# Kernel optimization log

Hardware: AMD Instinct MI355X
Metric: run time of the kernel (lower is better)

Reference implementation:

```python
import jax, jax.numpy as jnp
import numpy as np
from jax import lax


def setup_inputs() -> dict:
    key = jax.random.key(0)
    k1, k2 = jax.random.split(key)
    B, N, D = 4, 4096, 128
    f_s = jax.random.normal(k1, (B, N, D), dtype=jnp.float32)
    f_trans = jax.random.normal(k2, (B, N, D), dtype=jnp.float32)
    return {"f_s": f_s, "f_trans": f_trans}


def reference(f_s, f_trans):
    temp = 10.0
    eps = 1e-8
    B, N, D = f_s.shape
    # pairwise dot products, reused for cosine sim and for the logits ("all")
    dots = jnp.einsum('bnd,bmd->bnm', f_s, f_trans)  # [B,N,M]
    norm_s = jnp.linalg.norm(f_s, axis=-1)       # [B,N]
    norm_t = jnp.linalg.norm(f_trans, axis=-1)   # [B,M]
    # torch.cosine_similarity: dot / max(|x|*|y|, eps)
    sim = dots / jnp.maximum(norm_s[:, :, None] * norm_t[:, None, :], eps)
    # argmax over dim=1 (the N axis) -> index per (b, m)
    idx = jnp.argmax(sim, axis=1)  # [B,M] int
    # gather f_trans rows at those indices (detached in the original via numpy)
    pos_q_trans = lax.stop_gradient(
        jnp.take_along_axis(f_trans, idx[..., None], axis=1))  # [B,M,D]
    pos_logit = jnp.sum(f_s * pos_q_trans, axis=-1) / temp  # [B,N] (N==M)
    pos_exp = jnp.exp(pos_logit)
    # sum_m exp(<f_s_n, f_trans_m>/temp) without materializing [B,N,M,D]
    all_exp = jnp.sum(jnp.exp(dots / temp), axis=-1)  # [B,N]
    ratio = jnp.clip(pos_exp / all_exp, 1e-40)
    loss = jnp.mean(jnp.sum(-jnp.log(ratio), axis=-1) / N)
    return loss
```

## Files before the change

### kernel.cpp

```cpp
#include <hip/hip_runtime.h>
#include <math.h>

#define BB 4
#define NN 4096
#define DD 128
#define HS 8
#define NIT 8
#define QG 32

typedef __attribute__((ext_vector_type(8))) short bf16x8;
typedef __attribute__((ext_vector_type(4))) float f32x4;

__device__ __forceinline__ void mfma_16x16x32_bf16(f32x4& d, bf16x8 a, bf16x8 b) {
  asm volatile("v_mfma_f32_16x16x32_bf16 %0, %1, %2, %0" : "+v"(d) : "v"(a), "v"(b));
}

__device__ __forceinline__ void gload16(const void* g, void* lds) {
  __builtin_amdgcn_global_load_lds(
      (const __attribute__((address_space(1))) void*)g,
      (__attribute__((address_space(3))) void*)lds, 16, 0, 0);
}

__device__ __forceinline__ float vexp2(float x) {
  float r; asm("v_exp_f32 %0, %1" : "=v"(r) : "v"(x)); return r;
}

__device__ __forceinline__ unsigned short f2b(float x) {
  union { float f; unsigned u; } v; v.f = x;
  unsigned r = v.u + 0x7fffu + ((v.u >> 16) & 1u);
  return (unsigned short)(r >> 16);
}

__global__ __launch_bounds__(256) void k_prep(const float* __restrict__ fs,
                                              const float* __restrict__ ft,
                                              unsigned* __restrict__ outb,
                                              float* __restrict__ inv_norm) {
  int w = threadIdx.x >> 6, lane = threadIdx.x & 63;
  int row = blockIdx.x * 4 + w;
  bool is_s = row < BB * NN;
  const float* src = is_s ? fs + (size_t)row * DD
                          : ft + ((size_t)row - BB * NN) * DD;
  float2 v = ((const float2*)src)[lane];
  const float C = 0.14426950408889634f;
  float cx = is_s ? v.x : v.x * C;
  float cy = is_s ? v.y : v.y * C;
  outb[(size_t)row * 64 + lane] = ((unsigned)f2b(cy) << 16) | f2b(cx);
  if (is_s) {
    float s = v.x * v.x + v.y * v.y;
#pragma unroll
    for (int off = 32; off > 0; off >>= 1) s += __shfl_xor(s, off);
    if (lane == 0) inv_norm[row] = 1.0f / sqrtf(s);
  }
}

__global__ __launch_bounds__(256, 4) void k_main(const unsigned short* __restrict__ fsb,
                                                 const unsigned short* __restrict__ ftb,
                                                 const float* __restrict__ inv_norm,
                                                 float* __restrict__ psum,
                                                 float2* __restrict__ pmax) {
  __shared__ __align__(16) char smem[40960];
  float* psb = (float*)(smem + 32768);

  const int t = threadIdx.x;
  const int w = t >> 6, lane = t & 63;
  const int l15 = lane & 15, g = lane >> 4;
  const int bid = blockIdx.x;
  const int q = bid & 31, h = (bid >> 5) & 7, b = bid >> 8;
  const int m0 = q * 128 + w * 32;

  const int srcThr = ((t >> 4) << 8) + (((t & 15) ^ ((t >> 4) & 15)) << 4);
  const int ldsThr = w * 1024;

  const unsigned short* Ab = ftb + ((size_t)b * NN + m0) * DD;
  bf16x8 af[4][2];
#pragma unroll
  for (int kk = 0; kk < 4; kk++)
#pragma unroll
    for (int mf = 0; mf < 2; mf++)
      af[kk][mf] = *(const bf16x8*)(Ab + (mf * 16 + l15) * DD + kk * 32 + g * 8);

  const char* gB0 = (const char*)(fsb + ((size_t)b * NN + h * 512) * DD);
  const float* invb = inv_norm + (size_t)b * NN + h * 512;

  char* cb = smem;
  char* nb = smem + 16384;

#pragma unroll
  for (int p = 0; p < 4; p++)
    gload16(gB0 + p * 4096 + srcThr, cb + p * 4096 + ldsThr);

  float bkey[2][4];
#pragma unroll
  for (int mf = 0; mf < 2; mf++)
#pragma unroll
    for (int j = 0; j < 4; j++) bkey[mf][j] = 0.0f;

#pragma unroll 1
  for (int it = 0; it < NIT; ++it) {
    __syncthreads();
    if (it + 1 < NIT) {
      const char* gBn = gB0 + (it + 1) * 16384;
#pragma unroll
      for (int p = 0; p < 4; p++)
        gload16(gBn + p * 4096 + srcThr, nb + p * 4096 + ldsThr);
    }
    float svn[4];
#pragma unroll
    for (int fj = 0; fj < 4; fj++) svn[fj] = invb[it * 64 + fj * 16 + l15];

    f32x4 acc[2][4] = {};
#pragma unroll
    for (int kk = 0; kk < 4; kk++) {
      bf16x8 bf[4];
#pragma unroll
      for (int fj = 0; fj < 4; fj++)
        bf[fj] = *(const bf16x8*)(cb + (fj * 16 + l15) * 256 + (((kk * 4 + g) ^ l15) << 4));
#pragma unroll
      for (int mf = 0; mf < 2; mf++)
#pragma unroll
        for (int fj = 0; fj < 4; fj++)
          mfma_16x16x32_bf16(acc[mf][fj], af[kk][mf], bf[fj]);
    }

#pragma unroll
    for (int fj = 0; fj < 4; fj++) {
      float e0 = vexp2(acc[0][fj][0]), e1 = vexp2(acc[0][fj][1]);
      float e2 = vexp2(acc[0][fj][2]), e3 = vexp2(acc[0][fj][3]);
      float e4 = vexp2(acc[1][fj][0]), e5 = vexp2(acc[1][fj][1]);
      float e6 = vexp2(acc[1][fj][2]), e7 = vexp2(acc[1][fj][3]);
      float s = ((e0 + e1) + (e2 + e3)) + ((e4 + e5) + (e6 + e7));
      s += __shfl_xor(s, 16);
      s += __shfl_xor(s, 32);
      if (g == 0) psb[w * 512 + it * 64 + fj * 16 + l15] = s;
    }
    const unsigned codebase = (unsigned)((7 - it) << 2);
#pragma unroll
    for (int fj = 0; fj < 4; fj++) {
      const unsigned code = codebase | (unsigned)(3 - fj);
#pragma unroll
      for (int mf = 0; mf < 2; mf++)
#pragma unroll
        for (int j = 0; j < 4; j++) {
          float v = fmaf(acc[mf][fj][j], svn[fj], 4.0f);
          unsigned kb = (__float_as_uint(v) & 0xFFFFFFE0u) | code;
          bkey[mf][j] = fmaxf(bkey[mf][j], __uint_as_float(kb));
        }
    }
    char* tmp = cb; cb = nb; nb = tmp;
  }
  __syncthreads();

#pragma unroll
  for (int rr = 0; rr < 2; rr++) {
    int nl = rr * 256 + t;
    float s4 = (psb[nl] + psb[512 + nl]) + (psb[1024 + nl] + psb[1536 + nl]);
    psum[((size_t)(b * QG + q)) * NN + h * 512 + nl] = s4;
  }

#pragma unroll
  for (int mf = 0; mf < 2; mf++)
#pragma unroll
    for (int j = 0; j < 4; j++) {
      unsigned bits = __float_as_uint(bkey[mf][j]);
      unsigned code = bits & 31u;
      int itw = 7 - (int)(code >> 2);
      int fjw = 3 - (int)(code & 3u);
      int n = h * 512 + itw * 64 + fjw * 16 + l15;
      float vq = __uint_as_float(bits & 0xFFFFFFE0u);
#pragma unroll
      for (int off = 1; off <= 8; off <<= 1) {
        float ov = __shfl_xor(vq, off);
        int   on = __shfl_xor(n, off);
        if (ov > vq || (ov == vq && on < n)) { vq = ov; n = on; }
      }
      if (l15 == 0) {
        int m = m0 + mf * 16 + g * 4 + j;
        float2 pr; pr.x = vq; pr.y = __int_as_float(n);
        pmax[((size_t)b * NN + m) * HS + h] = pr;
      }
    }
}

__global__ __launch_bounds__(256) void k_post(const float* __restrict__ fs,
                                              const float* __restrict__ ft,
                                              const float* __restrict__ psum,
                                              const float2* __restrict__ pmax,
                                              float* __restrict__ blockpart) {
  __shared__ float part[4];
  int w = threadIdx.x >> 6, lane = threadIdx.x & 63;
  int row = blockIdx.x * 4 + w;
  int b = row >> 12, pn = row & (NN - 1);
  float v = -INFINITY; int i = 0x7fffffff;
  if (lane < HS) {
    float2 pm = pmax[(size_t)row * HS + lane];
    v = pm.x; i = __float_as_int(pm.y);
  }
#pragma unroll
  for (int off = 1; off <= 4; off <<= 1) {
    float ov = __shfl_xor(v, off);
    int   oi = __shfl_xor(i, off);
    if (ov > v || (ov == v && oi < i)) { v = ov; i = oi; }
  }
  int j = __shfl(i, 0);
  float tot = (lane < QG) ? psum[((size_t)(b * QG + lane)) * NN + pn] : 0.0f;
#pragma unroll
  for (int off = 1; off <= 16; off <<= 1) tot += __shfl_xor(tot, off);
  float2 a = ((const float2*)(fs + (size_t)row * DD))[lane];
  float2 c = ((const float2*)(ft + ((size_t)b * NN + j) * DD))[lane];
  float s = a.x * c.x + a.y * c.y;
#pragma unroll
  for (int off = 32; off > 0; off >>= 1) s += __shfl_xor(s, off);
  if (lane == 0) {
    float term = logf(tot) - s * 0.1f;
    part[w] = fminf(term, 92.103403719761827f);
  }
  __syncthreads();
  if (threadIdx.x == 0)
    blockpart[blockIdx.x] = part[0] + part[1] + part[2] + part[3];
}

__global__ __launch_bounds__(256) void k_final(const float* __restrict__ blockpart,
                                               float* __restrict__ out) {
  __shared__ float red[256];
  float s = 0.0f;
  for (int i = threadIdx.x; i < (BB * NN) / 4; i += 256) s += blockpart[i];
  red[threadIdx.x] = s;
  __syncthreads();
  for (int st = 128; st > 0; st >>= 1) {
    if (threadIdx.x < st) red[threadIdx.x] += red[threadIdx.x + st];
    __syncthreads();
  }
  if (threadIdx.x == 0) out[0] = red[0] * (1.0f / (BB * NN));
}

extern "C" void kernel_launch(void* const* d_in, const int* in_sizes, int n_in,
                              void* d_out, int out_size, void* d_ws, size_t ws_size,
                              hipStream_t stream) {
  const float* fs = (const float*)d_in[0];
  const float* ft = (const float*)d_in[1];
  float* out = (float*)d_out;

  const size_t NE = (size_t)BB * NN * DD;
  unsigned short* fsb = (unsigned short*)d_ws;
  unsigned short* ftb = fsb + NE;
  float*  inv_norm = (float*)(ftb + NE);
  float*  psum     = inv_norm + (size_t)BB * NN;
  float2* pmax     = (float2*)(psum + (size_t)BB * QG * NN);
  float*  blockpart = (float*)(pmax + (size_t)BB * NN * HS);

  k_prep<<<(2 * BB * NN) / 4, 256, 0, stream>>>(fs, ft, (unsigned*)fsb, inv_norm);
  k_main<<<BB * HS * QG, 256, 0, stream>>>(fsb, ftb, inv_norm, psum, pmax);
  k_post<<<(BB * NN) / 4, 256, 0, stream>>>(fs, ft, psum, pmax, blockpart);
  k_final<<<1, 256, 0, stream>>>(blockpart, out);
}
```

Measured before the change: 54.41 us.

## Split N range into 16 slices, drop LDS psum reduction, vectorize prep

The main kernel now splits the N dimension into 16 slices of 256 instead of 8 of 512, doubling the grid to 2048 blocks with half the iterations each. It raises the launch-bounds occupancy hint to 5 and shrinks LDS to 32 KB. Per-wave exp partial sums go straight to a [B,N,128] global buffer instead of being reduced through LDS, and the post kernel reduces 128 partials per row. The prep kernel uses float4 loads with both inputs per thread, and inverse norms are hoisted out of the loop. The trade is more parallelism and fewer barriers against more global partial-sum traffic and scattered strided writes.

```diff
diff --git a/kernel.cpp b/kernel.cpp
--- a/kernel.cpp
+++ b/kernel.cpp
@@ -4,12 +4,14 @@
 #define BB 4
 #define NN 4096
 #define DD 128
-#define HS 8
-#define NIT 8
+#define HS 16
+#define NIT 4
 #define QG 32
+#define NPS 128
 
 typedef __attribute__((ext_vector_type(8))) short bf16x8;
 typedef __attribute__((ext_vector_type(4))) float f32x4;
+typedef __attribute__((ext_vector_type(4))) unsigned short u16x4;
 
 __device__ __forceinline__ void mfma_16x16x32_bf16(f32x4& d, bf16x8 a, bf16x8 b) {
   asm volatile("v_mfma_f32_16x16x32_bf16 %0, %1, %2, %0" : "+v"(d) : "v"(a), "v"(b));
@@ -33,39 +35,36 @@
 
 __global__ __launch_bounds__(256) void k_prep(const float* __restrict__ fs,
                                               const float* __restrict__ ft,
-                                              unsigned* __restrict__ outb,
+                                              unsigned short* __restrict__ fsb,
+                                              unsigned short* __restrict__ ftb,
                                               float* __restrict__ inv_norm) {
-  int w = threadIdx.x >> 6, lane = threadIdx.x & 63;
-  int row = blockIdx.x * 4 + w;
-  bool is_s = row < BB * NN;
-  const float* src = is_s ? fs + (size_t)row * DD
-                          : ft + ((size_t)row - BB * NN) * DD;
-  float2 v = ((const float2*)src)[lane];
+  int i = blockIdx.x * 256 + threadIdx.x;
+  float4 a = ((const float4*)fs)[i];
+  float4 c = ((const float4*)ft)[i];
+  u16x4 oa; oa[0] = f2b(a.x); oa[1] = f2b(a.y); oa[2] = f2b(a.z); oa[3] = f2b(a.w);
+  ((u16x4*)fsb)[i] = oa;
   const float C = 0.14426950408889634f;
-  float cx = is_s ? v.x : v.x * C;
-  float cy = is_s ? v.y : v.y * C;
-  outb[(size_t)row * 64 + lane] = ((unsigned)f2b(cy) << 16) | f2b(cx);
-  if (is_s) {
-    float s = v.x * v.x + v.y * v.y;
-#pragma unroll
-    for (int off = 32; off > 0; off >>= 1) s += __shfl_xor(s, off);
-    if (lane == 0) inv_norm[row] = 1.0f / sqrtf(s);
-  }
-}
-
-__global__ __launch_bounds__(256, 4) void k_main(const unsigned short* __restrict__ fsb,
+  u16x4 oc; oc[0] = f2b(c.x * C); oc[1] = f2b(c.y * C);
+  oc[2] = f2b(c.z * C); oc[3] = f2b(c.w * C);
+  ((u16x4*)ftb)[i] = oc;
+  float s = a.x * a.x + a.y * a.y + a.z * a.z + a.w * a.w;
+#pragma unroll
+  for (int off = 1; off <= 16; off <<= 1) s += __shfl_xor(s, off);
+  if ((threadIdx.x & 31) == 0) inv_norm[i >> 5] = 1.0f / sqrtf(s);
+}
+
+__global__ __launch_bounds__(256, 5) void k_main(const unsigned short* __restrict__ fsb,
                                                  const unsigned short* __restrict__ ftb,
                                                  const float* __restrict__ inv_norm,
                                                  float* __restrict__ psum,
                                                  float2* __restrict__ pmax) {
-  __shared__ __align__(16) char smem[40960];
-  float* psb = (float*)(smem + 32768);
+  __shared__ __align__(16) char smem[32768];
 
   const int t = threadIdx.x;
   const int w = t >> 6, lane = t & 63;
   const int l15 = lane & 15, g = lane >> 4;
   const int bid = blockIdx.x;
-  const int q = bid & 31, h = (bid >> 5) & 7, b = bid >> 8;
+  const int q = bid & 31, h = (bid >> 5) & 15, b = bid >> 9;
   const int m0 = q * 128 + w * 32;
 
   const int srcThr = ((t >> 4) << 8) + (((t & 15) ^ ((t >> 4) & 15)) << 4);
@@ -79,8 +78,14 @@
     for (int mf = 0; mf < 2; mf++)
       af[kk][mf] = *(const bf16x8*)(Ab + (mf * 16 + l15) * DD + kk * 32 + g * 8);
 
-  const char* gB0 = (const char*)(fsb + ((size_t)b * NN + h * 512) * DD);
-  const float* invb = inv_norm + (size_t)b * NN + h * 512;
+  const char* gB0 = (const char*)(fsb + ((size_t)b * NN + h * 256) * DD);
+  const float* invb = inv_norm + (size_t)b * NN + h * 256;
+
+  float svn[NIT][4];
+#pragma unroll
+  for (int it = 0; it < NIT; it++)
+#pragma unroll
+    for (int fj = 0; fj < 4; fj++) svn[it][fj] = invb[it * 64 + fj * 16 + l15];
 
   char* cb = smem;
   char* nb = smem + 16384;
@@ -94,6 +99,8 @@
   for (int mf = 0; mf < 2; mf++)
 #pragma unroll
     for (int j = 0; j < 4; j++) bkey[mf][j] = 0.0f;
+
+  float* psumB = psum + (size_t)b * NN * NPS + (size_t)h * 256 * NPS + q * 4 + w;
 
 #pragma unroll 1
   for (int it = 0; it < NIT; ++it) {
@@ -104,10 +111,6 @@
       for (int p = 0; p < 4; p++)
         gload16(gBn + p * 4096 + srcThr, nb + p * 4096 + ldsThr);
     }
-    float svn[4];
-#pragma unroll
-    for (int fj = 0; fj < 4; fj++) svn[fj] = invb[it * 64 + fj * 16 + l15];
-
     f32x4 acc[2][4] = {};
 #pragma unroll
     for (int kk = 0; kk < 4; kk++) {
@@ -121,7 +124,6 @@
         for (int fj = 0; fj < 4; fj++)
           mfma_16x16x32_bf16(acc[mf][fj], af[kk][mf], bf[fj]);
     }
-
 #pragma unroll
     for (int fj = 0; fj < 4; fj++) {
       float e0 = vexp2(acc[0][fj][0]), e1 = vexp2(acc[0][fj][1]);
@@ -131,9 +133,9 @@
       float s = ((e0 + e1) + (e2 + e3)) + ((e4 + e5) + (e6 + e7));
       s += __shfl_xor(s, 16);
       s += __shfl_xor(s, 32);
-      if (g == 0) psb[w * 512 + it * 64 + fj * 16 + l15] = s;
-    }
-    const unsigned codebase = (unsigned)((7 - it) << 2);
+      if (g == 0) psumB[(it * 64 + fj * 16 + l15) * NPS] = s;
+    }
+    const unsigned codebase = (unsigned)((3 - it) << 2);
 #pragma unroll
     for (int fj = 0; fj < 4; fj++) {
       const unsigned code = codebase | (unsigned)(3 - fj);
@@ -141,32 +143,24 @@
       for (int mf = 0; mf < 2; mf++)
 #pragma unroll
         for (int j = 0; j < 4; j++) {
-          float v = fmaf(acc[mf][fj][j], svn[fj], 4.0f);
-          unsigned kb = (__float_as_uint(v) & 0xFFFFFFE0u) | code;
+          float v = fmaf(acc[mf][fj][j], svn[it][fj], 4.0f);
+          unsigned kb = (__float_as_uint(v) & 0xFFFFFFF0u) | code;
           bkey[mf][j] = fmaxf(bkey[mf][j], __uint_as_float(kb));
         }
     }
     char* tmp = cb; cb = nb; nb = tmp;
   }
-  __syncthreads();
-
-#pragma unroll
-  for (int rr = 0; rr < 2; rr++) {
-    int nl = rr * 256 + t;
-    float s4 = (psb[nl] + psb[512 + nl]) + (psb[1024 + nl] + psb[1536 + nl]);
-    psum[((size_t)(b * QG + q)) * NN + h * 512 + nl] = s4;
-  }
 
 #pragma unroll
   for (int mf = 0; mf < 2; mf++)
 #pragma unroll
     for (int j = 0; j < 4; j++) {
       unsigned bits = __float_as_uint(bkey[mf][j]);
-      unsigned code = bits & 31u;
-      int itw = 7 - (int)(code >> 2);
+      unsigned code = bits & 15u;
+      int itw = 3 - (int)(code >> 2);
       int fjw = 3 - (int)(code & 3u);
-      int n = h * 512 + itw * 64 + fjw * 16 + l15;
-      float vq = __uint_as_float(bits & 0xFFFFFFE0u);
+      int n = h * 256 + itw * 64 + fjw * 16 + l15;
+      float vq = __uint_as_float(bits & 0xFFFFFFF0u);
 #pragma unroll
       for (int off = 1; off <= 8; off <<= 1) {
         float ov = __shfl_xor(vq, off);
@@ -189,22 +183,23 @@
   __shared__ float part[4];
   int w = threadIdx.x >> 6, lane = threadIdx.x & 63;
   int row = blockIdx.x * 4 + w;
-  int b = row >> 12, pn = row & (NN - 1);
+  int b = row >> 12;
   float v = -INFINITY; int i = 0x7fffffff;
   if (lane < HS) {
     float2 pm = pmax[(size_t)row * HS + lane];
     v = pm.x; i = __float_as_int(pm.y);
   }
 #pragma unroll
-  for (int off = 1; off <= 4; off <<= 1) {
+  for (int off = 1; off <= 8; off <<= 1) {
     float ov = __shfl_xor(v, off);
     int   oi = __shfl_xor(i, off);
     if (ov > v || (ov == v && oi < i)) { v = ov; i = oi; }
   }
   int j = __shfl(i, 0);
-  float tot = (lane < QG) ? psum[((size_t)(b * QG + lane)) * NN + pn] : 0.0f;
-#pragma unroll
-  for (int off = 1; off <= 16; off <<= 1) tot += __shfl_xor(tot, off);
+  float2 qv = ((const float2*)(psum + (size_t)row * NPS))[lane];
+  float tot = qv.x + qv.y;
+#pragma unroll
+  for (int off = 1; off <= 32; off <<= 1) tot += __shfl_xor(tot, off);
   float2 a = ((const float2*)(fs + (size_t)row * DD))[lane];
   float2 c = ((const float2*)(ft + ((size_t)b * NN + j) * DD))[lane];
   float s = a.x * c.x + a.y * c.y;
@@ -245,10 +240,10 @@
   unsigned short* ftb = fsb + NE;
   float*  inv_norm = (float*)(ftb + NE);
   float*  psum     = inv_norm + (size_t)BB * NN;
-  float2* pmax     = (float2*)(psum + (size_t)BB * QG * NN);
+  float2* pmax     = (float2*)(psum + (size_t)BB * NN * NPS);
   float*  blockpart = (float*)(pmax + (size_t)BB * NN * HS);
 
-  k_prep<<<(2 * BB * NN) / 4, 256, 0, stream>>>(fs, ft, (unsigned*)fsb, inv_norm);
+  k_prep<<<(int)(NE / 4 / 256), 256, 0, stream>>>(fs, ft, fsb, ftb, inv_norm);
   k_main<<<BB * HS * QG, 256, 0, stream>>>(fsb, ftb, inv_norm, psum, pmax);
   k_post<<<(BB * NN) / 4, 256, 0, stream>>>(fs, ft, psum, pmax, blockpart);
   k_final<<<1, 256, 0, stream>>>(blockpart, out);
```

Result: slower. 97.36 us (+79.0%).
